# Kernel tuning notes

Hardware: AMD Instinct MI355X
Metric: run time of the kernel (lower is better)

## Reference

```python
import jax, jax.numpy as jnp
import numpy as np


def setup_inputs() -> dict:
    key = jax.random.key(0)
    B, C, A, P, N = 4, 1, 180, 384, 256
    sinogram = jax.random.normal(key, (B, C, A, P), dtype=jnp.float32)
    # projection angles uniformly covering [0, pi)
    thetas = jnp.linspace(0.0, np.pi, A, endpoint=False).astype(jnp.float32)
    # uniformly spaced detector positions centered at 0, unit spacing
    positions = jnp.arange(P, dtype=jnp.float32) - (P - 1) / 2.0
    return {"sinogram": sinogram, "thetas": thetas, "positions": positions, "image_size": N}


def reference(sinogram, thetas, positions, image_size):
    """Radon backprojection: image[y,x] = sum_a interp(sinogram[a], x*cos+y*sin)."""
    B, C, A, P = sinogram.shape
    N = image_size
    # pixel-center coordinates, image centered at origin (y axis pointing up)
    c = jnp.arange(N, dtype=sinogram.dtype) - (N - 1) / 2.0
    xs = c[None, :]          # [1, N]
    ys = -c[:, None]         # [N, 1]
    cos = jnp.cos(thetas)[:, None, None]  # [A, 1, 1]
    sin = jnp.sin(thetas)[:, None, None]
    t = xs[None] * cos + ys[None] * sin   # [A, N, N] detector coordinate per (angle, pixel)
    # fractional index into the (uniform) detector position grid
    dp = positions[1] - positions[0]
    f = (t - positions[0]) / dp           # [A, N, N]
    i0 = jnp.floor(f)
    w = f - i0                            # linear interpolation weight
    valid = (i0 >= 0) & (i0 <= P - 2)     # rays falling inside the detector
    i0c = jnp.clip(i0, 0, P - 2).astype(jnp.int32)
    idx = i0c.reshape(A, N * N)[None, None]          # [1, 1, A, N*N]
    v0 = jnp.take_along_axis(sinogram, idx, axis=3)  # [B, C, A, N*N]
    v1 = jnp.take_along_axis(sinogram, idx + 1, axis=3)
    wf = w.reshape(A, N * N)[None, None]
    vm = valid.reshape(A, N * N)[None, None]
    val = jnp.where(vm, v0 * (1.0 - wf) + v1 * wf, 0.0)
    return val.sum(axis=2).reshape(B, C, N, N)
```

## Files before the change

kernel.cpp:

```cpp
#include <hip/hip_runtime.h>
#include <hip/hip_fp16.h>
#include <cmath>


typedef __fp16 half2v __attribute__((ext_vector_type(2)));

__device__ __forceinline__ half2v as_h2(unsigned u) {
    union { unsigned u; half2v h; } x; x.u = u; return x.h;
}

__global__ __launch_bounds__(256) void radon_pack(
    const float* __restrict__ sino,
    const float* __restrict__ thetas,
    const float* __restrict__ positions,
    uint4* __restrict__ packed,
    float2* __restrict__ trig,
    int A, int P, int PES, int bstride)
{
    const int idx = blockIdx.x * 256 + threadIdx.x;
    const int a = idx / PES;
    const int j = idx - a * PES;
    if (a >= A) return;

    const float p0     = positions[0];
    const float inv_dp = 1.0f / (positions[1] - p0);
    if (j == 0) {
        float th = thetas[a];
        trig[a] = make_float2(cosf(th) * inv_dp, sinf(th) * inv_dp);
        if (a == 0) trig[A] = make_float2(-p0 * inv_dp, 0.0f);
    }

    uint4 e = make_uint4(0, 0, 0, 0);
    if (j >= 1 && j <= P - 1) {
        const float* s = sino + (size_t)a * P;
        unsigned* ep = (unsigned*)&e;
#pragma unroll
        for (int b = 0; b < 4; ++b) {
            const float* sb = s + (size_t)b * bstride;
            __half2 h = __floats2half2_rn(sb[j - 1], sb[j]);
            ep[b] = *(const unsigned*)&h;
        }
    }
    packed[(size_t)a * PES + j] = e;
}

__global__ __launch_bounds__(256) void radon_gather(
    const uint4* __restrict__ packed,
    const float2* __restrict__ trig,
    float* __restrict__ out,
    int A, int P, int PES, int N)
{
    const int tid = threadIdx.x;
    const int nn  = N * N;
    const int pix = blockIdx.x * 256 + tid;

    const int x = pix % N;
    const int y = pix / N;
    const float half = (float)(N - 1) * 0.5f;
    const float cx = (float)x - half;
    const float cy = half - (float)y;
    const float q0 = trig[A].x;

    float acc0 = 0.f, acc1 = 0.f, acc2 = 0.f, acc3 = 0.f;

#pragma unroll 4
    for (int a = 0; a < A; ++a) {
        float2 t  = trig[a];
        float f   = fmaf(cx, t.x, fmaf(cy, t.y, q0));
        float i0f = floorf(f);
        float w   = f - i0f;
        int   i0  = (int)i0f;
        int   j   = min(max(i0, -1), P - 1) + 1;

        half2v w2 = __builtin_amdgcn_cvt_pkrtz(1.0f - w, w);
        uint4 e = packed[(size_t)a * PES + j];
        acc0 = __builtin_amdgcn_fdot2(as_h2(e.x), w2, acc0, false);
        acc1 = __builtin_amdgcn_fdot2(as_h2(e.y), w2, acc1, false);
        acc2 = __builtin_amdgcn_fdot2(as_h2(e.z), w2, acc2, false);
        acc3 = __builtin_amdgcn_fdot2(as_h2(e.w), w2, acc3, false);
    }

    if (pix < nn) {
        float* op = out + pix;
        op[0]              = acc0;
        op[(size_t)nn]     = acc1;
        op[(size_t)2 * nn] = acc2;
        op[(size_t)3 * nn] = acc3;
    }
}

__global__ __launch_bounds__(256) void radon_direct_kernel(
    const float* __restrict__ sino,
    const float* __restrict__ thetas,
    const float* __restrict__ positions,
    float* __restrict__ out,
    int A, int P, int N, int BC)
{
    const int nn  = N * N;
    const int pix = blockIdx.x * blockDim.x + threadIdx.x;
    if (pix >= nn) return;
    const float p0     = positions[0];
    const float inv_dp = 1.0f / (positions[1] - p0);
    const int x = pix % N;
    const int y = pix / N;
    const float half = (float)(N - 1) * 0.5f;
    const float cx = (float)x - half;
    const float cy = half - (float)y;
    for (int b = 0; b < BC; ++b) {
        float acc = 0.0f;
        for (int a = 0; a < A; ++a) {
            float th = thetas[a];
            float f  = (cx * cosf(th) + cy * sinf(th) - p0) * inv_dp;
            float i0f = floorf(f);
            int i0 = (int)i0f;
            float w = f - i0f;
            float m = (i0 >= 0 && i0 <= P - 2) ? 1.0f : 0.0f;
            int ic = min(max(i0, 0), P - 2);
            const float* row = sino + ((size_t)b * A + a) * P + ic;
            acc = fmaf(m, fmaf(w, row[1] - row[0], row[0]), acc);
        }
        out[(size_t)b * nn + pix] = acc;
    }
}

extern "C" void kernel_launch(void* const* d_in, const int* in_sizes, int n_in,
                              void* d_out, int out_size, void* d_ws, size_t ws_size,
                              hipStream_t stream) {
    const float* sino      = (const float*)d_in[0];
    const float* thetas    = (const float*)d_in[1];
    const float* positions = (const float*)d_in[2];
    float* out             = (float*)d_out;

    const int A  = in_sizes[1];
    const int P  = in_sizes[2];
    const int BC = in_sizes[0] / (A * P);
    const int N  = (int)lroundf(sqrtf((float)(out_size / BC)));
    const int nn = N * N;
    const int bstride = A * P;

    const int PES = (P + 2 + 63) & ~63;

    const size_t packed_bytes = (size_t)A * PES * sizeof(uint4);
    const size_t trig_bytes   = (size_t)(A + 1) * sizeof(float2);
    const size_t need = packed_bytes + trig_bytes;

    const bool fast = (BC == 4) && (A <= 1024) && (P >= 2)
                   && ((nn & 255) == 0) && (ws_size >= need);

    if (fast) {
        uint4*  packed = (uint4*)d_ws;
        float2* trig   = (float2*)((char*)d_ws + packed_bytes);

        dim3 block(256);
        dim3 gpack(((unsigned)(A * PES) + 255) / 256);
        radon_pack<<<gpack, block, 0, stream>>>(
            sino, thetas, positions, packed, trig, A, P, PES, bstride);

        dim3 ggat(nn / 256);
        radon_gather<<<ggat, block, 0, stream>>>(
            packed, trig, out, A, P, PES, N);
    } else {
        dim3 block(256);
        dim3 grid((nn + 255) / 256);
        radon_direct_kernel<<<grid, block, 0, stream>>>(
            sino, thetas, positions, out, A, P, N, BC);
    }
}
```

Before: 86.74 us.

## Split angle loop into chunks across grid and reduce partial sums

The gather kernel now splits the angle dimension into 8 chunks along gridDim.y, and each block writes per-chunk partial sums to workspace. A new reduce kernel sums the chunks into the output with float4 loads. The aim is more parallelism, since the original grid had only 256 blocks for a GPU with many CUs. The cost is an extra kernel launch and extra global traffic for the partial buffer (8x4x65536 floats).

Measured after the change: 75.63 us. -12.8%, faster.

```diff
diff --git a/kernel.cpp b/kernel.cpp
--- a/kernel.cpp
+++ b/kernel.cpp
@@ -2,6 +2,8 @@
 #include <hip/hip_fp16.h>
 #include <cmath>
 
+
+#define ACHUNKS 8
 
 typedef __fp16 half2v __attribute__((ext_vector_type(2)));
 
@@ -44,15 +46,17 @@
     packed[(size_t)a * PES + j] = e;
 }
 
-__global__ __launch_bounds__(256) void radon_gather(
+__global__ __launch_bounds__(256) void radon_partial_pk(
     const uint4* __restrict__ packed,
     const float2* __restrict__ trig,
-    float* __restrict__ out,
-    int A, int P, int PES, int N)
+    float* __restrict__ part,
+    int A, int P, int PES, int N, int chunk)
 {
     const int tid = threadIdx.x;
     const int nn  = N * N;
     const int pix = blockIdx.x * 256 + tid;
+    const int a0  = blockIdx.y * chunk;
+    const int a1  = min(A, a0 + chunk);
 
     const int x = pix % N;
     const int y = pix / N;
@@ -64,7 +68,7 @@
     float acc0 = 0.f, acc1 = 0.f, acc2 = 0.f, acc3 = 0.f;
 
 #pragma unroll 4
-    for (int a = 0; a < A; ++a) {
+    for (int a = a0; a < a1; ++a) {
         float2 t  = trig[a];
         float f   = fmaf(cx, t.x, fmaf(cy, t.y, q0));
         float i0f = floorf(f);
@@ -81,12 +85,27 @@
     }
 
     if (pix < nn) {
-        float* op = out + pix;
-        op[0]              = acc0;
-        op[(size_t)nn]     = acc1;
-        op[(size_t)2 * nn] = acc2;
-        op[(size_t)3 * nn] = acc3;
+        float* pp = part + (size_t)blockIdx.y * 4 * nn + pix;
+        pp[0]              = acc0;
+        pp[(size_t)nn]     = acc1;
+        pp[(size_t)2 * nn] = acc2;
+        pp[(size_t)3 * nn] = acc3;
     }
+}
+
+__global__ __launch_bounds__(256) void radon_reduce_kernel(
+    const float4* __restrict__ part,
+    float4* __restrict__ out,
+    int BN4, int nchunks)
+{
+    int i = blockIdx.x * blockDim.x + threadIdx.x;
+    if (i >= BN4) return;
+    float4 s = make_float4(0.f, 0.f, 0.f, 0.f);
+    for (int c = 0; c < nchunks; ++c) {
+        float4 v = part[(size_t)c * BN4 + i];
+        s.x += v.x; s.y += v.y; s.z += v.z; s.w += v.w;
+    }
+    out[i] = s;
 }
 
 __global__ __launch_bounds__(256) void radon_direct_kernel(
@@ -138,27 +157,35 @@
     const int nn = N * N;
     const int bstride = A * P;
 
-    const int PES = (P + 2 + 63) & ~63;
+    const int PES   = (P + 2 + 63) & ~63;
+    const int chunk = (A + ACHUNKS - 1) / ACHUNKS;
 
+    const size_t part_bytes   = (size_t)ACHUNKS * 4 * nn * sizeof(float);
     const size_t packed_bytes = (size_t)A * PES * sizeof(uint4);
     const size_t trig_bytes   = (size_t)(A + 1) * sizeof(float2);
-    const size_t need = packed_bytes + trig_bytes;
+    const size_t need = part_bytes + packed_bytes + trig_bytes;
 
     const bool fast = (BC == 4) && (A <= 1024) && (P >= 2)
-                   && ((nn & 255) == 0) && (ws_size >= need);
+                   && ((nn & 255) == 0) && ((nn & 3) == 0) && (ws_size >= need);
 
     if (fast) {
-        uint4*  packed = (uint4*)d_ws;
-        float2* trig   = (float2*)((char*)d_ws + packed_bytes);
+        float*  part   = (float*)d_ws;
+        uint4*  packed = (uint4*)((char*)d_ws + part_bytes);
+        float2* trig   = (float2*)((char*)d_ws + part_bytes + packed_bytes);
 
         dim3 block(256);
         dim3 gpack(((unsigned)(A * PES) + 255) / 256);
         radon_pack<<<gpack, block, 0, stream>>>(
             sino, thetas, positions, packed, trig, A, P, PES, bstride);
 
-        dim3 ggat(nn / 256);
-        radon_gather<<<ggat, block, 0, stream>>>(
-            packed, trig, out, A, P, PES, N);
+        dim3 gpart(nn / 256, ACHUNKS);
+        radon_partial_pk<<<gpart, block, 0, stream>>>(
+            packed, trig, part, A, P, PES, N, chunk);
+
+        const int BN4 = nn;
+        dim3 gred((BN4 + 255) / 256);
+        radon_reduce_kernel<<<gred, block, 0, stream>>>(
+            (const float4*)part, (float4*)out, BN4, ACHUNKS);
     } else {
         dim3 block(256);
         dim3 grid((nn + 255) / 256);
```

## Split angle loop across grid.y chunks with atomic accumulation

Applied to the files above, without the earlier changes.

The gather kernel now splits the angle loop into 8 chunks along grid.y. Each block adds its partial sums to the output with atomicAdd, which multiplies the number of blocks beyond one per pixel tile. To support this, the pack kernel also zeroes the output. Pack conversion now uses a vector float2 load and round-toward-zero packing. The change trades more parallelism and occupancy for extra atomic traffic, a zeroing pass, nondeterministic summation order, and slightly different fp16 rounding.

Result: faster. 72.66 us (-16.2%).

```diff
diff --git a/kernel.cpp b/kernel.cpp
--- a/kernel.cpp
+++ b/kernel.cpp
@@ -2,6 +2,8 @@
 #include <hip/hip_fp16.h>
 #include <cmath>
 
+
+#define ACHUNKS 8
 
 typedef __fp16 half2v __attribute__((ext_vector_type(2)));
 
@@ -9,17 +11,20 @@
     union { unsigned u; half2v h; } x; x.u = u; return x.h;
 }
 
-__global__ __launch_bounds__(256) void radon_pack(
+__global__ __launch_bounds__(256) void radon_pack_zero(
     const float* __restrict__ sino,
     const float* __restrict__ thetas,
     const float* __restrict__ positions,
     uint4* __restrict__ packed,
     float2* __restrict__ trig,
-    int A, int P, int PES, int bstride)
+    float4* __restrict__ out4,
+    int A, int P, int PES, int bstride, int nout4)
 {
-    const int idx = blockIdx.x * 256 + threadIdx.x;
-    const int a = idx / PES;
-    const int j = idx - a * PES;
+    const int gidx = blockIdx.x * 256 + threadIdx.x;
+    if (gidx < nout4) out4[gidx] = make_float4(0.f, 0.f, 0.f, 0.f);
+
+    const int a = gidx / PES;
+    const int j = gidx - a * PES;
     if (a >= A) return;
 
     const float p0     = positions[0];
@@ -32,27 +37,30 @@
 
     uint4 e = make_uint4(0, 0, 0, 0);
     if (j >= 1 && j <= P - 1) {
-        const float* s = sino + (size_t)a * P;
+        const float* s = sino + (size_t)a * P + (j - 1);
         unsigned* ep = (unsigned*)&e;
 #pragma unroll
         for (int b = 0; b < 4; ++b) {
-            const float* sb = s + (size_t)b * bstride;
-            __half2 h = __floats2half2_rn(sb[j - 1], sb[j]);
-            ep[b] = *(const unsigned*)&h;
+            float2 v = *(const float2*)(s + (size_t)b * bstride);
+            half2v h = __builtin_amdgcn_cvt_pkrtz(v.x, v.y);
+            union { half2v h; unsigned u; } cvt; cvt.h = h;
+            ep[b] = cvt.u;
         }
     }
     packed[(size_t)a * PES + j] = e;
 }
 
-__global__ __launch_bounds__(256) void radon_gather(
+__global__ __launch_bounds__(256) void radon_gather_at(
     const uint4* __restrict__ packed,
     const float2* __restrict__ trig,
     float* __restrict__ out,
-    int A, int P, int PES, int N)
+    int A, int P, int PES, int N, int chunk)
 {
     const int tid = threadIdx.x;
     const int nn  = N * N;
     const int pix = blockIdx.x * 256 + tid;
+    const int a0  = blockIdx.y * chunk;
+    const int a1  = min(A, a0 + chunk);
 
     const int x = pix % N;
     const int y = pix / N;
@@ -64,7 +72,7 @@
     float acc0 = 0.f, acc1 = 0.f, acc2 = 0.f, acc3 = 0.f;
 
 #pragma unroll 4
-    for (int a = 0; a < A; ++a) {
+    for (int a = a0; a < a1; ++a) {
         float2 t  = trig[a];
         float f   = fmaf(cx, t.x, fmaf(cy, t.y, q0));
         float i0f = floorf(f);
@@ -82,10 +90,10 @@
 
     if (pix < nn) {
         float* op = out + pix;
-        op[0]              = acc0;
-        op[(size_t)nn]     = acc1;
-        op[(size_t)2 * nn] = acc2;
-        op[(size_t)3 * nn] = acc3;
+        atomicAdd(op,                  acc0);
+        atomicAdd(op + (size_t)nn,     acc1);
+        atomicAdd(op + (size_t)2 * nn, acc2);
+        atomicAdd(op + (size_t)3 * nn, acc3);
     }
 }
 
@@ -138,7 +146,9 @@
     const int nn = N * N;
     const int bstride = A * P;
 
-    const int PES = (P + 2 + 63) & ~63;
+    const int PES   = (P + 2 + 63) & ~63;
+    const int chunk = (A + ACHUNKS - 1) / ACHUNKS;
+    const int nout4 = nn;
 
     const size_t packed_bytes = (size_t)A * PES * sizeof(uint4);
     const size_t trig_bytes   = (size_t)(A + 1) * sizeof(float2);
@@ -152,13 +162,15 @@
         float2* trig   = (float2*)((char*)d_ws + packed_bytes);
 
         dim3 block(256);
-        dim3 gpack(((unsigned)(A * PES) + 255) / 256);
-        radon_pack<<<gpack, block, 0, stream>>>(
-            sino, thetas, positions, packed, trig, A, P, PES, bstride);
+        const unsigned gp = (unsigned)(((size_t)A * PES > (size_t)nout4
+                                        ? (size_t)A * PES : (size_t)nout4) + 255) / 256;
+        radon_pack_zero<<<dim3(gp), block, 0, stream>>>(
+            sino, thetas, positions, packed, trig, (float4*)out,
+            A, P, PES, bstride, nout4);
 
-        dim3 ggat(nn / 256);
-        radon_gather<<<ggat, block, 0, stream>>>(
-            packed, trig, out, A, P, PES, N);
+        dim3 gpart(nn / 256, ACHUNKS);
+        radon_gather_at<<<gpart, block, 0, stream>>>(
+            packed, trig, out, A, P, PES, N, chunk);
     } else {
         dim3 block(256);
         dim3 grid((nn + 255) / 256);
```
